# Optimization experiments

Hardware: AMD Instinct MI355X
Metric: run time of the kernel (lower is better)

The kernel has to match this reference:

```python
import jax, jax.numpy as jnp
import numpy as np
from jax import lax


def setup_inputs() -> dict:
    key = jax.random.key(0)
    k0, k1, k2, k3 = jax.random.split(key, 4)
    B, C, H, W = 16, 64, 192, 192
    K = 3
    x0 = jax.random.normal(k0, (B, C, H, W), dtype=jnp.float32)
    d = jax.random.normal(k1, (B, C), dtype=jnp.float32)
    w1 = jax.random.normal(k2, (C, C), dtype=jnp.float32) * 0.05
    w2 = jax.random.normal(k3, (C * K * K, C), dtype=jnp.float32) * 0.05
    return {"x0": x0, "d": d, "w1": w1, "w2": w2}


def reference(x0, d, w1, w2):
    b, c, h, w = x0.shape
    k = int(round((w2.shape[0] // c) ** 0.5))  # kernel_size
    # kernel-generating MLP: Linear(C,C,bias=False) -> LeakyReLU(0.1) -> Linear(C,C*k*k,bias=False)
    hid = jax.nn.leaky_relu(d @ w1.T, negative_slope=0.1)          # (B, C)
    ker = (hid @ w2.T).reshape(b * c, 1, k, k)                      # (B*C, 1, k, k)
    pad = (k - 1) // 2
    # per-(batch,channel) dynamic depthwise conv: groups = B*C
    out = lax.conv_general_dilated(
        x0.reshape(1, b * c, h, w),
        ker,
        window_strides=(1, 1),
        padding=[(pad, pad), (pad, pad)],
        dimension_numbers=("NCHW", "OIHW", "NCHW"),
        feature_group_count=b * c,
    )
    return out.reshape(b, c, h, w)
```

## Files before the change

### kernel.cpp

```cpp
#include <hip/hip_runtime.h>


#define BB 16
#define CC 64
#define HH 192
#define WW 192
#define KERLEN (CC * 9)
#define QW (WW / 4)
#define ROWS 32
#define RIN (ROWS + 2)
#define ROWB (WW * 4)
#define TILEB (RIN * ROWB)
#define STAGEB (7 * 4096)
#define TILES (HH / ROWS)

typedef float f4 __attribute__((ext_vector_type(4)));

__global__ __launch_bounds__(256) void gen_kernels(
    const float* __restrict__ d,
    const float* __restrict__ w1,
    const float* __restrict__ w2,
    float* __restrict__ ker)
{
    __shared__ float dd[CC];
    __shared__ float hid[CC];
    const int b = blockIdx.x;
    const int t = threadIdx.x;

    if (t < CC) dd[t] = d[b * CC + t];
    __syncthreads();

    if (t < CC) {
        const float* w1r = w1 + t * CC;
        float acc = 0.f;
        #pragma unroll 8
        for (int m = 0; m < CC; ++m) acc += dd[m] * w1r[m];
        hid[t] = acc > 0.f ? acc : 0.1f * acc;
    }
    __syncthreads();

    for (int o = t; o < KERLEN; o += 256) {
        const float* w2r = w2 + o * CC;
        float acc = 0.f;
        #pragma unroll 8
        for (int k = 0; k < CC; ++k) acc += hid[k] * w2r[k];
        ker[b * KERLEN + o] = acc;
    }
}

__device__ __forceinline__ void gload_lds16(const float* g, float* l) {
    __builtin_amdgcn_global_load_lds(
        (const __attribute__((address_space(1))) unsigned int*)g,
        (__attribute__((address_space(3))) unsigned int*)l,
        16, 0, 0);
}

__global__ __launch_bounds__(256, 5) void dconv3x3_v5(
    const float* __restrict__ x,
    const float* __restrict__ ker,
    float* __restrict__ out)
{
    __shared__ __align__(16) float lds[STAGEB / 4];

    const int blk  = blockIdx.x;
    const int bc   = blk / TILES;
    const int tile = blk - bc * TILES;
    const int r0   = tile * ROWS;

    const float* __restrict__ xp = x   + (size_t)bc * HH * WW;
    float* __restrict__       op = out + (size_t)bc * HH * WW;

    const float* kp = ker + bc * 9;
    const float k00 = kp[0], k01 = kp[1], k02 = kp[2];
    const float k10 = kp[3], k11 = kp[4], k12 = kp[5];
    const float k20 = kp[6], k21 = kp[7], k22 = kp[8];

    const int t = threadIdx.x;

    #pragma unroll
    for (int i = 0; i < 7; ++i) {
        const int idx  = i * 4096 + t * 16;
        const int j    = idx / ROWB;
        const int colb = idx - j * ROWB;
        int srow = r0 - 1 + j;
        srow = srow < 0 ? 0 : (srow > HH - 1 ? HH - 1 : srow);
        gload_lds16(xp + srow * WW + (colb >> 2), lds + (idx >> 2));
    }
    asm volatile("s_waitcnt vmcnt(0)" ::: "memory");
    __syncthreads();

    const f4 zero = {0.f, 0.f, 0.f, 0.f};

    #pragma unroll
    for (int k2 = 0; k2 < 3; ++k2) {
        const int task = t + k2 * 256;
        const int pr   = task / QW;
        const int q    = task - pr * QW;
        const int lr0  = pr * 2;

        const bool hasL = (q > 0);
        const bool hasR = (q < QW - 1);
        const int  offL = hasL ? -1 : 0;
        const int  offR = hasR ?  4 : 0;

        f4    c[4];
        float l[4], r[4];

        #pragma unroll
        for (int dj = 0; dj < 4; ++dj) {
            const int g = r0 + lr0 - 1 + dj;
            const float* p = lds + (lr0 + dj) * WW + q * 4;
            const f4 v     = *(const f4*)p;
            const float lv = p[offL];
            const float rv = p[offR];
            const bool ok  = (unsigned)g < (unsigned)HH;
            c[dj] = ok ? v : zero;
            l[dj] = (ok && hasL) ? lv : 0.f;
            r[dj] = (ok && hasR) ? rv : 0.f;
        }

        #pragma unroll
        for (int i = 0; i < 2; ++i) {
            const f4 ca = c[i], cb = c[i + 1], cd = c[i + 2];
            const float la = l[i], lb = l[i + 1], lc = l[i + 2];
            const float ra = r[i], rb = r[i + 1], rc = r[i + 2];

            f4 o;
            o.x = k00 * la   + k01 * ca.x + k02 * ca.y
                + k10 * lb   + k11 * cb.x + k12 * cb.y
                + k20 * lc   + k21 * cd.x + k22 * cd.y;
            o.y = k00 * ca.x + k01 * ca.y + k02 * ca.z
                + k10 * cb.x + k11 * cb.y + k12 * cb.z
                + k20 * cd.x + k21 * cd.y + k22 * cd.z;
            o.z = k00 * ca.y + k01 * ca.z + k02 * ca.w
                + k10 * cb.y + k11 * cb.z + k12 * cb.w
                + k20 * cd.y + k21 * cd.z + k22 * cd.w;
            o.w = k00 * ca.z + k01 * ca.w + k02 * ra
                + k10 * cb.z + k11 * cb.w + k12 * rb
                + k20 * cd.z + k21 * cd.w + k22 * rc;

            __builtin_nontemporal_store(
                o, (f4*)(op + (size_t)(r0 + lr0 + i) * WW + q * 4));
        }
    }
}

extern "C" void kernel_launch(void* const* d_in, const int* in_sizes, int n_in,
                              void* d_out, int out_size, void* d_ws, size_t ws_size,
                              hipStream_t stream) {
    const float* x0 = (const float*)d_in[0];
    const float* d  = (const float*)d_in[1];
    const float* w1 = (const float*)d_in[2];
    const float* w2 = (const float*)d_in[3];
    float* out = (float*)d_out;
    float* ker = (float*)d_ws;

    gen_kernels<<<BB, 256, 0, stream>>>(d, w1, w2, ker);
    dconv3x3_v5<<<BB * CC * TILES, 256, 0, stream>>>(x0, ker, out);
}
```

Before: 272.2 us.

## Make conv blocks persistent per channel with double-buffered LDS row windows

Each block now handles a whole (batch, channel) image instead of one 32-row tile. It walks eight 24-row output tiles, prefetching the next input window into a second LDS buffer while computing the current one. The aim is to overlap global-to-LDS loads with compute and to cut the number of blocks and the redundant per-block kernel-weight loads. In exchange the grid shrinks to 1024 blocks, occupancy drops to 4 blocks per SIMD set, and the explicit vmcnt wait is gone, so correctness depends on the barrier ordering the async LDS loads.

```diff
diff --git a/kernel.cpp b/kernel.cpp
--- a/kernel.cpp
+++ b/kernel.cpp
@@ -7,12 +7,12 @@
 #define WW 192
 #define KERLEN (CC * 9)
 #define QW (WW / 4)
-#define ROWS 32
-#define RIN (ROWS + 2)
+#define OUTR 24
+#define NTIL 8
 #define ROWB (WW * 4)
-#define TILEB (RIN * ROWB)
-#define STAGEB (7 * 4096)
-#define TILES (HH / ROWS)
+#define CHUNKS 5
+#define WINB (CHUNKS * 4096)
+#define WINF (WINB / 4)
 
 typedef float f4 __attribute__((ext_vector_type(4)));
 
@@ -48,24 +48,33 @@
     }
 }
 
-__device__ __forceinline__ void gload_lds16(const float* g, float* l) {
-    __builtin_amdgcn_global_load_lds(
-        (const __attribute__((address_space(1))) unsigned int*)g,
-        (__attribute__((address_space(3))) unsigned int*)l,
-        16, 0, 0);
+__device__ __forceinline__ void stage_window(const float* __restrict__ xp,
+                                             float* __restrict__ buf,
+                                             int wstart, int t) {
+    #pragma unroll
+    for (int i = 0; i < CHUNKS; ++i) {
+        const int off = i * 4096 + t * 16;
+        const int row = off / ROWB;
+        const int col = off - row * ROWB;
+        int srow = wstart + row;
+        srow = srow < 0 ? 0 : (srow > HH - 1 ? HH - 1 : srow);
+        __builtin_amdgcn_global_load_lds(
+            (const __attribute__((address_space(1))) unsigned int*)
+                (xp + srow * WW + (col >> 2)),
+            (__attribute__((address_space(3))) unsigned int*)(buf + (off >> 2)),
+            16, 0, 0);
+    }
 }
 
-__global__ __launch_bounds__(256, 5) void dconv3x3_v5(
+__global__ __launch_bounds__(256, 4) void dconv3x3_v7(
     const float* __restrict__ x,
     const float* __restrict__ ker,
     float* __restrict__ out)
 {
-    __shared__ __align__(16) float lds[STAGEB / 4];
+    __shared__ __align__(16) float lds[2][WINF];
 
-    const int blk  = blockIdx.x;
-    const int bc   = blk / TILES;
-    const int tile = blk - bc * TILES;
-    const int r0   = tile * ROWS;
+    const int bc = blockIdx.x;
+    const int t  = threadIdx.x;
 
     const float* __restrict__ xp = x   + (size_t)bc * HH * WW;
     float* __restrict__       op = out + (size_t)bc * HH * WW;
@@ -75,73 +84,62 @@
     const float k10 = kp[3], k11 = kp[4], k12 = kp[5];
     const float k20 = kp[6], k21 = kp[7], k22 = kp[8];
 
-    const int t = threadIdx.x;
-
-    #pragma unroll
-    for (int i = 0; i < 7; ++i) {
-        const int idx  = i * 4096 + t * 16;
-        const int j    = idx / ROWB;
-        const int colb = idx - j * ROWB;
-        int srow = r0 - 1 + j;
-        srow = srow < 0 ? 0 : (srow > HH - 1 ? HH - 1 : srow);
-        gload_lds16(xp + srow * WW + (colb >> 2), lds + (idx >> 2));
-    }
-    asm volatile("s_waitcnt vmcnt(0)" ::: "memory");
+    stage_window(xp, lds[0], -1, t);
     __syncthreads();
 
-    const f4 zero = {0.f, 0.f, 0.f, 0.f};
+    for (int tt = 0; tt < NTIL; ++tt) {
+        if (tt < NTIL - 1)
+            stage_window(xp, lds[(tt + 1) & 1], (tt + 1) * OUTR - 1, t);
 
-    #pragma unroll
-    for (int k2 = 0; k2 < 3; ++k2) {
-        const int task = t + k2 * 256;
-        const int pr   = task / QW;
-        const int q    = task - pr * QW;
-        const int lr0  = pr * 2;
-
-        const bool hasL = (q > 0);
-        const bool hasR = (q < QW - 1);
-        const int  offL = hasL ? -1 : 0;
-        const int  offR = hasR ?  4 : 0;
-
-        f4    c[4];
-        float l[4], r[4];
+        const float* __restrict__ buf = lds[tt & 1];
+        const int out0 = tt * OUTR;
 
         #pragma unroll
-        for (int dj = 0; dj < 4; ++dj) {
-            const int g = r0 + lr0 - 1 + dj;
-            const float* p = lds + (lr0 + dj) * WW + q * 4;
-            const f4 v     = *(const f4*)p;
-            const float lv = p[offL];
-            const float rv = p[offR];
-            const bool ok  = (unsigned)g < (unsigned)HH;
-            c[dj] = ok ? v : zero;
-            l[dj] = (ok && hasL) ? lv : 0.f;
-            r[dj] = (ok && hasR) ? rv : 0.f;
+        for (int k = 0; k < 5; ++k) {
+            const int task = t + k * 256;
+            if (task < OUTR * QW) {
+                const int rl = task / QW;
+                const int q  = task - rl * QW;
+                const bool hasL = (q > 0);
+                const bool hasR = (q < QW - 1);
+                const int  offL = hasL ? -1 : 0;
+                const int  offR = hasR ?  4 : 0;
+                const int  gr   = out0 + rl;
+
+                f4 c[3]; float l[3], r[3];
+                const f4 zero = {0.f, 0.f, 0.f, 0.f};
+                #pragma unroll
+                for (int dj = 0; dj < 3; ++dj) {
+                    const int gin = gr - 1 + dj;
+                    const float* p = buf + (rl + dj) * WW + q * 4;
+                    const f4 v     = *(const f4*)p;
+                    const float lv = p[offL];
+                    const float rv = p[offR];
+                    const bool ok  = (unsigned)gin < (unsigned)HH;
+                    c[dj] = ok ? v : zero;
+                    l[dj] = (ok && hasL) ? lv : 0.f;
+                    r[dj] = (ok && hasR) ? rv : 0.f;
+                }
+
+                f4 o;
+                o.x = k00 * l[0]   + k01 * c[0].x + k02 * c[0].y
+                    + k10 * l[1]   + k11 * c[1].x + k12 * c[1].y
+                    + k20 * l[2]   + k21 * c[2].x + k22 * c[2].y;
+                o.y = k00 * c[0].x + k01 * c[0].y + k02 * c[0].z
+                    + k10 * c[1].x + k11 * c[1].y + k12 * c[1].z
+                    + k20 * c[2].x + k21 * c[2].y + k22 * c[2].z;
+                o.z = k00 * c[0].y + k01 * c[0].z + k02 * c[0].w
+                    + k10 * c[1].y + k11 * c[1].z + k12 * c[1].w
+                    + k20 * c[2].y + k21 * c[2].z + k22 * c[2].w;
+                o.w = k00 * c[0].z + k01 * c[0].w + k02 * r[0]
+                    + k10 * c[1].z + k11 * c[1].w + k12 * r[1]
+                    + k20 * c[2].z + k21 * c[2].w + k22 * r[2];
+
+                __builtin_nontemporal_store(o, (f4*)(op + (size_t)gr * WW + q * 4));
+            }
         }
 
-        #pragma unroll
-        for (int i = 0; i < 2; ++i) {
-            const f4 ca = c[i], cb = c[i + 1], cd = c[i + 2];
-            const float la = l[i], lb = l[i + 1], lc = l[i + 2];
-            const float ra = r[i], rb = r[i + 1], rc = r[i + 2];
-
-            f4 o;
-            o.x = k00 * la   + k01 * ca.x + k02 * ca.y
-                + k10 * lb   + k11 * cb.x + k12 * cb.y
-                + k20 * lc   + k21 * cd.x + k22 * cd.y;
-            o.y = k00 * ca.x + k01 * ca.y + k02 * ca.z
-                + k10 * cb.x + k11 * cb.y + k12 * cb.z
-                + k20 * cd.x + k21 * cd.y + k22 * cd.z;
-            o.z = k00 * ca.y + k01 * ca.z + k02 * ca.w
-                + k10 * cb.y + k11 * cb.z + k12 * cb.w
-                + k20 * cd.y + k21 * cd.z + k22 * cd.w;
-            o.w = k00 * ca.z + k01 * ca.w + k02 * ra
-                + k10 * cb.z + k11 * cb.w + k12 * rb
-                + k20 * cd.z + k21 * cd.w + k22 * rc;
-
-            __builtin_nontemporal_store(
-                o, (f4*)(op + (size_t)(r0 + lr0 + i) * WW + q * 4));
-        }
+        __syncthreads();
     }
 }
 
@@ -156,5 +154,5 @@
     float* ker = (float*)d_ws;
 
     gen_kernels<<<BB, 256, 0, stream>>>(d, w1, w2, ker);
-    dconv3x3_v5<<<BB * CC * TILES, 256, 0, stream>>>(x0, ker, out);
+    dconv3x3_v7<<<BB * CC, 256, 0, stream>>>(x0, ker, out);
 }
```

After: 281.2 us. 1.03x slower.
